# Kernel optimization log

Hardware: AMD Instinct MI355X
Metric: run time of the kernel (lower is better)

The kernel has to match this reference:

```python
import jax, jax.numpy as jnp
import numpy as np
import math

B, S, E, H = 2, 2048, 1024, 16
D = E // H          # d_k = 64 = n_qubits_per_head
F = 1024            # ffn_dim; MUST equal E for the original mixing to broadcast
LN_EPS = 1e-5


def _layernorm(x, g, b):
    m = jnp.mean(x, axis=-1, keepdims=True)
    v = jnp.var(x, axis=-1, keepdims=True)
    return (x - m) / jnp.sqrt(v + LN_EPS) * g + b


def _circuit_expvals(x):
    # Closed form of the variational circuit: RY(x_i) on wire i, RZ(theta_i),
    # CNOT chain (i -> i+1), measure PauliZ on each wire.
    # RZ is diagonal (no effect on Z probs); CNOT chain makes bit_i the XOR of
    # bits 0..i, so <Z_i> = prod_{j<=i} cos(x_j).
    return jnp.cumprod(jnp.cos(x), axis=-1)


def setup_inputs() -> dict:
    key = jax.random.key(0)
    ks = jax.random.split(key, 18)
    sc = 0.02
    inp = {
        "x": jax.random.normal(ks[0], (B, S, E), jnp.float32),
        "mask": jnp.ones((B, S), jnp.int32),
        "wq": jax.random.normal(ks[1], (E, E), jnp.float32) * sc,
        "wk": jax.random.normal(ks[2], (E, E), jnp.float32) * sc,
        "wv": jax.random.normal(ks[3], (E, E), jnp.float32) * sc,
        "wo": jax.random.normal(ks[4], (E, E), jnp.float32) * sc,
        "attn_param": jax.random.normal(ks[5], (D,), jnp.float32),   # RZ angles (no effect on expvals)
        "attn_qw": jnp.float32(0.5),
        "w1": jax.random.normal(ks[6], (E, F), jnp.float32) * sc,
        "b1": jnp.zeros((F,), jnp.float32),
        "w2": jax.random.normal(ks[7], (F, E), jnp.float32) * sc,
        "b2": jnp.zeros((E,), jnp.float32),
        "ffn_param": jax.random.normal(ks[8], (E,), jnp.float32),    # RZ angles (no effect on expvals)
        "ffn_qw": jnp.float32(0.5),
        "ln1_g": jnp.ones((E,), jnp.float32),
        "ln1_b": jnp.zeros((E,), jnp.float32),
        "ln2_g": jnp.ones((E,), jnp.float32),
        "ln2_b": jnp.zeros((E,), jnp.float32),
    }
    return inp


def reference(x, mask, wq, wk, wv, wo, attn_param, attn_qw,
              w1, b1, w2, b2, ffn_param, ffn_qw,
              ln1_g, ln1_b, ln2_g, ln2_b):
    b, s, _ = x.shape
    # ---- quantum attention sublayer (dropout inactive / eval mode) ----
    q = (x @ wq).reshape(b, s, H, D).transpose(0, 2, 1, 3)  # [b,h,s,d]
    k = (x @ wk).reshape(b, s, H, D).transpose(0, 2, 1, 3)
    v = (x @ wv).reshape(b, s, H, D).transpose(0, 2, 1, 3)
    scores = jnp.einsum("bhqd,bhkd->bhqk", q, k) / math.sqrt(D)
    scores = jnp.where(mask[:, None, None, :] == 0, -jnp.inf, scores)
    attn = jax.nn.softmax(scores, axis=-1)
    classical = jnp.einsum("bhqk,bhkd->bhqd", attn, v)
    quantum = _circuit_expvals(q)                             # [b,h,s,d]
    wgt = jax.nn.sigmoid(attn_qw)
    out = wgt * quantum + (1.0 - wgt) * classical
    attn_out = out.transpose(0, 2, 1, 3).reshape(b, s, E) @ wo
    x1 = _layernorm(x + attn_out, ln1_g, ln1_b)
    # ---- quantum feed-forward sublayer ----
    classical2 = jax.nn.relu(x1 @ w1 + b1)                    # [b,s,F]
    quantum2 = _circuit_expvals(x1)                           # [b,s,E] (E==F)
    wgt2 = jax.nn.sigmoid(ffn_qw)
    h = wgt2 * quantum2 + (1.0 - wgt2) * classical2
    ffn_out = h @ w2 + b2
    return _layernorm(x1 + ffn_out, ln2_g, ln2_b)
```

## Files before the change

### kernel.cpp

```cpp
#include <hip/hip_runtime.h>
#include <hip/hip_bf16.h>
#include <cmath>
#include <cstdint>


typedef __bf16 bf16_t;
typedef __bf16 bf16x8 __attribute__((ext_vector_type(8)));
typedef float f32x4 __attribute__((ext_vector_type(4)));
typedef unsigned short u16x4 __attribute__((ext_vector_type(4)));

#define DEV_INLINE __device__ __forceinline__
#define MB 1048576

DEV_INLINE void gload16(const void* g, void* lds) {
  __builtin_amdgcn_global_load_lds(
      (const __attribute__((address_space(1))) unsigned int*)g,
      (__attribute__((address_space(3))) unsigned int*)lds, 16, 0, 0);
}

DEV_INLINE unsigned short bf16_bits(float f) {
  bf16_t b = (bf16_t)f;
  return __builtin_bit_cast(unsigned short, b);
}

#define BAR_PRE_LGKM asm volatile("s_waitcnt lgkmcnt(0)" ::: "memory")
#define BAR_PRE_VM8 asm volatile("s_waitcnt vmcnt(8)" ::: "memory")
#define BAR_PRE_VM4 asm volatile("s_waitcnt vmcnt(4)" ::: "memory")
#define RAW_BAR                 \
  __builtin_amdgcn_s_barrier(); \
  asm volatile("" ::: "memory")

__global__ __launch_bounds__(256) void prep_kernel(
    const float* __restrict__ x, const float* __restrict__ wq,
    const float* __restrict__ wk, const float* __restrict__ wv,
    const float* __restrict__ wo, const float* __restrict__ w1,
    const float* __restrict__ w2, bf16_t* __restrict__ xc,
    bf16_t* __restrict__ wqkvT, bf16_t* __restrict__ wT3) {
  __shared__ bf16_t t[32][33];
  const int bid = blockIdx.x;
  if (bid < 2048) {
    const size_t i0 = ((size_t)bid * 256 + threadIdx.x) * 8;
    bf16x8 v;
#pragma unroll
    for (int j = 0; j < 8; ++j) v[j] = (bf16_t)x[i0 + j];
    *(bf16x8*)(xc + i0) = v;
    return;
  }
  const int grp = (bid - 2048) / 3072;
  const int tcb = (bid - 2048) - grp * 3072;
  const int mi = tcb >> 10;
  const float* src;
  bf16_t* dst;
  if (grp == 0) {
    src = (mi == 0) ? wq : (mi == 1) ? wk : wv;
    dst = wqkvT;
  } else {
    src = (mi == 0) ? wo : (mi == 1) ? w1 : w2;
    dst = wT3;
  }
  const int rem = tcb & 1023;
  const int bx = (rem & 31) * 32, by = (rem >> 5) * 32;
  const int tx = threadIdx.x & 31, ty = threadIdx.x >> 5;
#pragma unroll
  for (int i = 0; i < 4; ++i)
    t[ty + i * 8][tx] = (bf16_t)src[(size_t)(by + ty + i * 8) * 1024 + bx + tx];
  __syncthreads();
#pragma unroll
  for (int i = 0; i < 4; ++i)
    dst[(size_t)(mi * 1024 + bx + ty + i * 8) * 1024 + by + tx] = t[tx][ty + i * 8];
}

DEV_INLINE void stage_tile(const char* __restrict__ G, char* ldsT, int k0b,
                           int wid, int lane) {
#pragma unroll
  for (int t = 0; t < 4; ++t) {
    const int plin = t * 8192 + wid * 1024 + lane * 16;
    const int p = plin ^ ((((unsigned)plin >> 7) & 7) << 4);
    gload16(G + (size_t)(p >> 7) * 2048 + k0b + (p & 127),
            ldsT + t * 8192 + wid * 1024);
  }
}

DEV_INLINE void compute_tile(const char* lds_tile, int wm, int wn, int quad,
                             int tc, f32x4 (&acc)[8][4]) {
  const char* Ab = lds_tile;
  const char* Bb = lds_tile + 32768;
#pragma unroll
  for (int ks = 0; ks < 2; ++ks) {
    const int colb = ks * 64 + quad * 16;
    bf16x8 bfv[4];
#pragma unroll
    for (int j = 0; j < 4; ++j) {
      const int r = wn + j * 16 + tc;
      bfv[j] = *(const bf16x8*)(Bb + ((r * 128 + colb) ^ ((r & 7) << 4)));
    }
#pragma unroll
    for (int ih = 0; ih < 2; ++ih) {
      bf16x8 af[4];
#pragma unroll
      for (int i = 0; i < 4; ++i) {
        const int r = wm + (ih * 4 + i) * 16 + tc;
        af[i] = *(const bf16x8*)(Ab + ((r * 128 + colb) ^ ((r & 7) << 4)));
      }
      __builtin_amdgcn_s_setprio(1);
#pragma unroll
      for (int i = 0; i < 4; ++i)
#pragma unroll
        for (int j = 0; j < 4; ++j)
          acc[ih * 4 + i][j] = __builtin_amdgcn_mfma_f32_16x16x32_bf16(
              af[i], bfv[j], acc[ih * 4 + i][j], 0, 0, 0);
      __builtin_amdgcn_s_setprio(0);
    }
  }
}

__global__ __launch_bounds__(512, 2) void qkvvt8_kernel(
    const bf16_t* __restrict__ xc, const bf16_t* __restrict__ wqkvT,
    bf16_t* __restrict__ qb, bf16_t* __restrict__ kb,
    bf16_t* __restrict__ vTb) {
  __shared__ __align__(16) char lds[131072];
  const int tid = threadIdx.x, wid = tid >> 6, lane = tid & 63;
  const int quad = lane >> 4, tc = lane & 15;
  const int bid = blockIdx.x;
  const int isqk = (bid < 128);
  int m0, n0;
  const char *A, *B;
  if (isqk) {
    m0 = (bid >> 3) * 256;
    n0 = (bid & 7) * 256;
    A = (const char*)(xc + (size_t)m0 * 1024);
    B = (const char*)(wqkvT + (size_t)n0 * 1024);
  } else {
    const int t2 = bid - 128;
    m0 = (t2 >> 4) * 256;
    n0 = (t2 & 15) * 256;
    A = (const char*)(wqkvT + (size_t)(2 * 1024 * 1024) + (size_t)m0 * 1024);
    B = (const char*)(xc + (size_t)n0 * 1024);
  }
  const int wm = (wid >> 2) * 128, wn = (wid & 3) * 64;

  f32x4 acc[8][4] = {};

  stage_tile(A, lds, 0, wid, lane);
  stage_tile(B, lds + 32768, 0, wid, lane);
  stage_tile(A, lds + 65536, 128, wid, lane);
  stage_tile(B, lds + 98304, 128, wid, lane);
  BAR_PRE_VM8;
  RAW_BAR;

  for (int it = 0; it < 7; ++it) {
    const int k0b = it * 256 + 256;
    compute_tile(lds, wm, wn, quad, tc, acc);
    BAR_PRE_LGKM;
    RAW_BAR;
    stage_tile(A, lds, k0b, wid, lane);
    stage_tile(B, lds + 32768, k0b, wid, lane);
    BAR_PRE_VM8;
    RAW_BAR;
    compute_tile(lds + 65536, wm, wn, quad, tc, acc);
    BAR_PRE_LGKM;
    RAW_BAR;
    stage_tile(A, lds + 65536, k0b + 128, wid, lane);
    stage_tile(B, lds + 98304, k0b + 128, wid, lane);
    BAR_PRE_VM8;
    RAW_BAR;
  }
  compute_tile(lds, wm, wn, quad, tc, acc);
  asm volatile("s_waitcnt vmcnt(0)" ::: "memory");
  BAR_PRE_LGKM;
  RAW_BAR;
  compute_tile(lds + 65536, wm, wn, quad, tc, acc);

#pragma unroll
  for (int i = 0; i < 8; ++i) {
#pragma unroll
    for (int j = 0; j < 4; ++j) {
      const int row0 = m0 + wm + i * 16 + quad * 4;
      const int col = n0 + wn + j * 16 + tc;
      if (isqk) {
        const int part = col >> 10, e = col & 1023, hh = e >> 6, d = e & 63;
        bf16_t* dst = part ? kb : qb;
#pragma unroll
        for (int r = 0; r < 4; ++r) {
          const int row = row0 + r;
          const int b = row >> 11, s = row & 2047;
          dst[((size_t)(b * 16 + hh) * 2048 + s) * 64 + d] = (bf16_t)acc[i][j][r];
        }
      } else {
        const int b = col >> 11, s = col & 2047;
#pragma unroll
        for (int r = 0; r < 4; ++r) {
          vTb[((size_t)(b * 1024 + row0 + r)) * 2048 + s] = (bf16_t)acc[i][j][r];
        }
      }
    }
  }
}

enum { EPI_WO = 2, EPI_W1 = 3, EPI_W2 = 4 };

DEV_INLINE void stage128(const char* __restrict__ G, char* ldsT, int k0b,
                         int wid, int lane) {
#pragma unroll
  for (int t = 0; t < 4; ++t) {
    const int plin = t * 4096 + wid * 1024 + lane * 16;
    const int p = plin ^ ((((unsigned)plin >> 7) & 7) << 4);
    gload16(G + (size_t)(p >> 7) * 2048 + k0b + (p & 127),
            ldsT + t * 4096 + wid * 1024);
  }
}

DEV_INLINE void compute128(const char* lds_tile, int wm, int wn, int quad,
                           int tc, f32x4 (&acc)[4][4]) {
  const char* Ab = lds_tile;
  const char* Bb = lds_tile + 16384;
#pragma unroll
  for (int ks = 0; ks < 2; ++ks) {
    const int colb = ks * 64 + quad * 16;
    bf16x8 bfv[4];
#pragma unroll
    for (int j = 0; j < 4; ++j) {
      const int r = wn + j * 16 + tc;
      bfv[j] = *(const bf16x8*)(Bb + ((r * 128 + colb) ^ ((r & 7) << 4)));
    }
#pragma unroll
    for (int ih = 0; ih < 2; ++ih) {
      bf16x8 af[2];
#pragma unroll
      for (int i = 0; i < 2; ++i) {
        const int r = wm + (ih * 2 + i) * 16 + tc;
        af[i] = *(const bf16x8*)(Ab + ((r * 128 + colb) ^ ((r & 7) << 4)));
      }
      __builtin_amdgcn_s_setprio(1);
#pragma unroll
      for (int i = 0; i < 2; ++i)
#pragma unroll
        for (int j = 0; j < 4; ++j)
          acc[ih * 2 + i][j] = __builtin_amdgcn_mfma_f32_16x16x32_bf16(
              af[i], bfv[j], acc[ih * 2 + i][j], 0, 0, 0);
      __builtin_amdgcn_s_setprio(0);
    }
  }
}

template <int EPI>
__global__ __launch_bounds__(256, 2) void gemm8_kernel(
    const bf16_t* __restrict__ A, const bf16_t* __restrict__ Bt,
    void* __restrict__ o0, const float* __restrict__ auxf,
    const bf16_t* __restrict__ auxb, const float* __restrict__ bias,
    const float* __restrict__ scal) {
  __shared__ __align__(16) char lds[65536];
  const int tid = threadIdx.x, wid = tid >> 6, lane = tid & 63;
  const int quad = lane >> 4, tc = lane & 15;
  const int bid = blockIdx.x;
  const int g = (bid & 7) * 32 + (bid >> 3);
  const int m0 = (g >> 3) * 128, n0 = (g & 7) * 128;
  const char* Ag = (const char*)A + (size_t)m0 * 2048;
  const char* Bg = (const char*)Bt + (size_t)n0 * 2048;
  const int wm = (wid >> 1) * 64, wn = (wid & 1) * 64;

  f32x4 acc[4][4] = {};

  stage128(Ag, lds, 0, wid, lane);
  stage128(Bg, lds + 16384, 0, wid, lane);
  stage128(Ag, lds + 32768, 128, wid, lane);
  stage128(Bg, lds + 49152, 128, wid, lane);
  BAR_PRE_VM4;
  RAW_BAR;

  for (int it = 0; it < 7; ++it) {
    const int k0b = it * 256 + 256;
    compute128(lds, wm, wn, quad, tc, acc);
    BAR_PRE_LGKM;
    RAW_BAR;
    stage128(Ag, lds, k0b, wid, lane);
    stage128(Bg, lds + 16384, k0b, wid, lane);
    BAR_PRE_VM4;
    RAW_BAR;
    compute128(lds + 32768, wm, wn, quad, tc, acc);
    BAR_PRE_LGKM;
    RAW_BAR;
    stage128(Ag, lds + 32768, k0b + 128, wid, lane);
    stage128(Bg, lds + 49152, k0b + 128, wid, lane);
    BAR_PRE_VM4;
    RAW_BAR;
  }
  compute128(lds, wm, wn, quad, tc, acc);
  asm volatile("s_waitcnt vmcnt(0)" ::: "memory");
  BAR_PRE_LGKM;
  RAW_BAR;
  compute128(lds + 32768, wm, wn, quad, tc, acc);

  float wsig = 0.f;
  if (EPI == EPI_W1) wsig = 1.f / (1.f + __expf(-scal[0]));

#pragma unroll
  for (int i = 0; i < 4; ++i) {
#pragma unroll
    for (int j = 0; j < 4; ++j) {
      const int row0 = m0 + wm + i * 16 + quad * 4;
      const int col = n0 + wn + j * 16 + tc;
      if (EPI == EPI_WO) {
#pragma unroll
        for (int r = 0; r < 4; ++r) {
          const int row = row0 + r;
          ((float*)o0)[(size_t)row * 1024 + col] =
              acc[i][j][r] + auxf[(size_t)row * 1024 + col];
        }
      } else if (EPI == EPI_W1) {
#pragma unroll
        for (int r = 0; r < 4; ++r) {
          const int row = row0 + r;
          float c = fmaxf(acc[i][j][r] + bias[col], 0.f);
          const float qv = (float)auxb[(size_t)row * 1024 + col];
          ((bf16_t*)o0)[(size_t)row * 1024 + col] =
              (bf16_t)(wsig * qv + (1.f - wsig) * c);
        }
      } else {
#pragma unroll
        for (int r = 0; r < 4; ++r) {
          const int row = row0 + r;
          ((float*)o0)[(size_t)row * 1024 + col] =
              acc[i][j][r] + bias[col] + (float)auxb[(size_t)row * 1024 + col];
        }
      }
    }
  }
}

__global__ __launch_bounds__(256) void attn_kernel(
    const bf16_t* __restrict__ q, const bf16_t* __restrict__ k,
    const bf16_t* __restrict__ vT, const float* __restrict__ aqw,
    bf16_t* __restrict__ out) {
  constexpr int S = 2048, LDK = 72;
  __shared__ __align__(16) bf16_t Ks[64 * LDK];
  __shared__ __align__(16) bf16_t Vs[64 * LDK];
  __shared__ __align__(16) bf16_t Ps[4][32 * LDK];
  __shared__ bf16_t Ql[128 * LDK];
  __shared__ float segp[128][4];

  const int tid = threadIdx.x, w = tid >> 6, lane = tid & 63;
  const int quad = lane >> 4, tc = lane & 15;
  const int bh = blockIdx.y, q0 = blockIdx.x * 128;
  const bf16_t* qg = q + ((size_t)bh * S + q0) * 64;
  const bf16_t* kg = k + (size_t)bh * S * 64;
  const bf16_t* vg = vT + (size_t)bh * 64 * S;

  const int strow = tid >> 2, stcol = (tid & 3) * 16;

  bf16x8 pk0 = *(const bf16x8*)(kg + (size_t)strow * 64 + stcol);
  bf16x8 pk1 = *(const bf16x8*)(kg + (size_t)strow * 64 + stcol + 8);
  bf16x8 pv0 = *(const bf16x8*)(vg + (size_t)strow * S + stcol);
  bf16x8 pv1 = *(const bf16x8*)(vg + (size_t)strow * S + stcol + 8);

  {
    float c[2][16];
    const int ss = tid & 3;
#pragma unroll
    for (int pass = 0; pass < 2; ++pass) {
      const int rr = pass * 64 + (tid >> 2);
      const bf16_t* qr = qg + rr * 64 + ss * 16;
      float p = 1.f;
#pragma unroll
      for (int j2 = 0; j2 < 16; ++j2) {
        c[pass][j2] = __cosf((float)qr[j2]);
        p *= c[pass][j2];
      }
      segp[rr][ss] = p;
    }
    __syncthreads();
#pragma unroll
    for (int pass = 0; pass < 2; ++pass) {
      const int rr = pass * 64 + (tid >> 2);
      float pre = 1.f;
      for (int u = 0; u < ss; ++u) pre *= segp[rr][u];
#pragma unroll
      for (int j2 = 0; j2 < 16; ++j2) {
        pre *= c[pass][j2];
        Ql[rr * LDK + ss * 16 + j2] = (bf16_t)pre;
      }
    }
  }

  bf16x8 aq[2][2];
#pragma unroll
  for (int qs = 0; qs < 2; ++qs) {
    const int qrow = w * 32 + qs * 16 + tc;
#pragma unroll
    for (int ks = 0; ks < 2; ++ks) {
      bf16x8 t = *(const bf16x8*)(qg + qrow * 64 + ks * 32 + quad * 8);
#pragma unroll
      for (int e = 0; e < 8; ++e) t[e] = (bf16_t)((float)t[e] * 0.18033688f);
      aq[qs][ks] = t;
    }
  }

  float lacc[2] = {0.f, 0.f};
  f32x4 o[2][4] = {};
  bf16_t* Pw = Ps[w];

  for (int kt = 0; kt < S; kt += 64) {
    __syncthreads();
    *(bf16x8*)&Ks[strow * LDK + stcol] = pk0;
    *(bf16x8*)&Ks[strow * LDK + stcol + 8] = pk1;
    *(bf16x8*)&Vs[strow * LDK + stcol] = pv0;
    *(bf16x8*)&Vs[strow * LDK + stcol + 8] = pv1;
    if (kt + 64 < S) {
      const int nk = kt + 64;
      pk0 = *(const bf16x8*)(kg + (size_t)(nk + strow) * 64 + stcol);
      pk1 = *(const bf16x8*)(kg + (size_t)(nk + strow) * 64 + stcol + 8);
      pv0 = *(const bf16x8*)(vg + (size_t)strow * S + nk + stcol);
      pv1 = *(const bf16x8*)(vg + (size_t)strow * S + nk + stcol + 8);
    }
    __syncthreads();

    f32x4 sf[2][4] = {};
#pragma unroll
    for (int ks = 0; ks < 2; ++ks) {
#pragma unroll
      for (int nt = 0; nt < 4; ++nt) {
        bf16x8 ak = *(const bf16x8*)&Ks[(nt * 16 + tc) * LDK + ks * 32 + quad * 8];
        sf[0][nt] = __builtin_amdgcn_mfma_f32_16x16x32_bf16(ak, aq[0][ks], sf[0][nt], 0, 0, 0);
        sf[1][nt] = __builtin_amdgcn_mfma_f32_16x16x32_bf16(ak, aq[1][ks], sf[1][nt], 0, 0, 0);
      }
    }

#pragma unroll
    for (int qs = 0; qs < 2; ++qs) {
#pragma unroll
      for (int nt = 0; nt < 4; ++nt) {
        u16x4 pk;
        float ps = 0.f;
#pragma unroll
        for (int r = 0; r < 4; ++r) {
          const float p = __builtin_amdgcn_exp2f(sf[qs][nt][r]);
          ps += p;
          pk[r] = bf16_bits(p);
        }
        lacc[qs] += ps;
        *(u16x4*)&Pw[(qs * 16 + tc) * LDK + nt * 16 + quad * 4] = pk;
      }
    }
    asm volatile("s_waitcnt lgkmcnt(0)" ::: "memory");

#pragma unroll
    for (int ks = 0; ks < 2; ++ks) {
      bf16x8 ap0 = *(const bf16x8*)&Pw[tc * LDK + ks * 32 + quad * 8];
      bf16x8 ap1 = *(const bf16x8*)&Pw[(16 + tc) * LDK + ks * 32 + quad * 8];
#pragma unroll
      for (int j = 0; j < 4; ++j) {
        bf16x8 bv = *(const bf16x8*)&Vs[(j * 16 + tc) * LDK + ks * 32 + quad * 8];
        o[0][j] = __builtin_amdgcn_mfma_f32_16x16x32_bf16(ap0, bv, o[0][j], 0, 0, 0);
        o[1][j] = __builtin_amdgcn_mfma_f32_16x16x32_bf16(ap1, bv, o[1][j], 0, 0, 0);
      }
    }
  }

#pragma unroll
  for (int qs = 0; qs < 2; ++qs) {
    lacc[qs] += __shfl_xor(lacc[qs], 16, 64);
    lacc[qs] += __shfl_xor(lacc[qs], 32, 64);
  }

  const float wsig = 1.f / (1.f + __expf(-aqw[0]));
  const int b = bh >> 4, h = bh & 15;
#pragma unroll
  for (int qs = 0; qs < 2; ++qs) {
#pragma unroll
    for (int r = 0; r < 4; ++r) {
      const int lr = quad * 4 + r;
      const float linv = 1.f / __shfl(lacc[qs], lr, 64);
      const int lrow = w * 32 + qs * 16 + lr;
      const int sg = q0 + lrow;
#pragma unroll
      for (int j = 0; j < 4; ++j) {
        const int d = j * 16 + tc;
        const float cl = o[qs][j][r] * linv;
        const float qv = (float)Ql[lrow * LDK + d];
        out[((size_t)(b * 2048 + sg)) * 1024 + h * 64 + d] =
            (bf16_t)(wsig * qv + (1.f - wsig) * cl);
      }
    }
  }
}

__global__ __launch_bounds__(256) void ln1scan_kernel(
    const float* __restrict__ res, const float* __restrict__ g,
    const float* __restrict__ bta, bf16_t* __restrict__ x1,
    bf16_t* __restrict__ q2) {
  const int row = blockIdx.x;
  const int tid = threadIdx.x, w = tid >> 6, lane = tid & 63;
  f32x4 v = *(const f32x4*)&res[(size_t)row * 1024 + tid * 4];
  float s = v[0] + v[1] + v[2] + v[3];
  float sq = v[0] * v[0] + v[1] * v[1] + v[2] * v[2] + v[3] * v[3];
#pragma unroll
  for (int off = 32; off >= 1; off >>= 1) {
    s += __shfl_xor(s, off, 64);
    sq += __shfl_xor(sq, off, 64);
  }
  __shared__ float rs[4], rq[4], wtot[4];
  if (lane == 0) {
    rs[w] = s;
    rq[w] = sq;
  }
  __syncthreads();
  s = rs[0] + rs[1] + rs[2] + rs[3];
  sq = rq[0] + rq[1] + rq[2] + rq[3];
  const float mean = s * (1.f / 1024.f);
  const float var = fmaxf(sq * (1.f / 1024.f) - mean * mean, 0.f);
  const float rstd = rsqrtf(var + 1e-5f);

  const f32x4 gv = *(const f32x4*)&g[tid * 4];
  const f32x4 bv = *(const f32x4*)&bta[tid * 4];
  float c[4], p = 1.f;
  u16x4 xb;
#pragma unroll
  for (int i = 0; i < 4; ++i) {
    const float y = (v[i] - mean) * rstd * gv[i] + bv[i];
    const bf16_t yb = (bf16_t)y;
    xb[i] = __builtin_bit_cast(unsigned short, yb);
    c[i] = __cosf((float)yb);
    p *= c[i];
  }
  *(u16x4*)&x1[(size_t)row * 1024 + tid * 4] = xb;

  float ip = p;
#pragma unroll
  for (int off = 1; off < 64; off <<= 1) {
    const float t = __shfl_up(ip, off, 64);
    if (lane >= off) ip *= t;
  }
  if (lane == 63) wtot[w] = ip;
  __syncthreads();
  float carry = 1.f;
  for (int u = 0; u < w; ++u) carry *= wtot[u];
  float run = __shfl_up(ip, 1, 64);
  if (lane == 0) run = 1.f;
  run *= carry;
  u16x4 qv;
#pragma unroll
  for (int i = 0; i < 4; ++i) {
    run *= c[i];
    qv[i] = bf16_bits(run);
  }
  *(u16x4*)&q2[(size_t)row * 1024 + tid * 4] = qv;
}

__global__ __launch_bounds__(256) void ln2_kernel(
    const float* __restrict__ res, const float* __restrict__ g,
    const float* __restrict__ bta, float* __restrict__ out) {
  const int row = blockIdx.x;
  const int tid = threadIdx.x, w = tid >> 6, lane = tid & 63;
  f32x4 v = *(const f32x4*)&res[(size_t)row * 1024 + tid * 4];
  float s = v[0] + v[1] + v[2] + v[3];
  float sq = v[0] * v[0] + v[1] * v[1] + v[2] * v[2] + v[3] * v[3];
#pragma unroll
  for (int off = 32; off >= 1; off >>= 1) {
    s += __shfl_xor(s, off, 64);
    sq += __shfl_xor(sq, off, 64);
  }
  __shared__ float rs[4], rq[4];
  if (lane == 0) {
    rs[w] = s;
    rq[w] = sq;
  }
  __syncthreads();
  s = rs[0] + rs[1] + rs[2] + rs[3];
  sq = rq[0] + rq[1] + rq[2] + rq[3];
  const float mean = s * (1.f / 1024.f);
  const float var = fmaxf(sq * (1.f / 1024.f) - mean * mean, 0.f);
  const float rstd = rsqrtf(var + 1e-5f);
  const f32x4 gv = *(const f32x4*)&g[tid * 4];
  const f32x4 bv = *(const f32x4*)&bta[tid * 4];
  f32x4 y;
#pragma unroll
  for (int i = 0; i < 4; ++i) y[i] = (v[i] - mean) * rstd * gv[i] + bv[i];
  *(f32x4*)&out[(size_t)row * 1024 + tid * 4] = y;
}

extern "C" void kernel_launch(void* const* d_in, const int* in_sizes, int n_in,
                              void* d_out, int out_size, void* d_ws,
                              size_t ws_size, hipStream_t stream) {
  (void)in_sizes;
  (void)n_in;
  (void)out_size;
  (void)ws_size;
  const float* x = (const float*)d_in[0];
  const float* wq = (const float*)d_in[2];
  const float* wk = (const float*)d_in[3];
  const float* wv = (const float*)d_in[4];
  const float* wo = (const float*)d_in[5];
  const float* attn_qw = (const float*)d_in[7];
  const float* w1 = (const float*)d_in[8];
  const float* b1 = (const float*)d_in[9];
  const float* w2 = (const float*)d_in[10];
  const float* b2 = (const float*)d_in[11];
  const float* ffn_qw = (const float*)d_in[13];
  const float* ln1_g = (const float*)d_in[14];
  const float* ln1_b = (const float*)d_in[15];
  const float* ln2_g = (const float*)d_in[16];
  const float* ln2_b = (const float*)d_in[17];

  char* ws = (char*)d_ws;
  char* wsout = (char*)d_out;
  bf16_t* wT3 = (bf16_t*)(ws + 0);
  bf16_t* wqkvT = (bf16_t*)(ws + 6 * MB);
  bf16_t* xc = (bf16_t*)(ws + 12 * MB);
  bf16_t* qb = (bf16_t*)(ws + 20 * MB);
  bf16_t* aout = (bf16_t*)(ws + 6 * MB);
  float* res = (float*)(ws + 14 * MB);
  bf16_t* x1 = (bf16_t*)(ws + 6 * MB);
  float* res2 = (float*)(ws + 14 * MB);
  bf16_t* kb = (bf16_t*)(wsout + 0);
  bf16_t* vTb = (bf16_t*)(wsout + 8 * MB);
  bf16_t* q2 = (bf16_t*)(wsout + 0);
  bf16_t* hbuf = (bf16_t*)(wsout + 8 * MB);

  const dim3 tb(256);

  prep_kernel<<<8192, tb, 0, stream>>>(x, wq, wk, wv, wo, w1, w2, xc, wqkvT, wT3);

  qkvvt8_kernel<<<192, dim3(512), 0, stream>>>(xc, wqkvT, qb, kb, vTb);

  attn_kernel<<<dim3(16, 32), tb, 0, stream>>>(qb, kb, vTb, attn_qw, aout);

  gemm8_kernel<EPI_WO><<<256, tb, 0, stream>>>(
      aout, wT3, res, x, nullptr, nullptr, nullptr);

  ln1scan_kernel<<<4096, tb, 0, stream>>>(res, ln1_g, ln1_b, x1, q2);

  gemm8_kernel<EPI_W1><<<256, tb, 0, stream>>>(
      x1, wT3 + 1024 * 1024, hbuf, nullptr, q2, b1, ffn_qw);

  gemm8_kernel<EPI_W2><<<256, tb, 0, stream>>>(
      hbuf, wT3 + 2 * 1024 * 1024, res2, nullptr, x1, b2, nullptr);

  ln2_kernel<<<4096, tb, 0, stream>>>(res2, ln2_g, ln2_b, (float*)d_out);
}
```

Measured before the change: 266.9 us.

## Split attention blocks into eight waves of 16 rows and compute cumprod via shuffles

```diff
diff --git a/kernel.cpp b/kernel.cpp
--- a/kernel.cpp
+++ b/kernel.cpp
@@ -328,16 +328,14 @@
   }
 }
 
-__global__ __launch_bounds__(256) void attn_kernel(
+__global__ __launch_bounds__(512, 4) void attn_kernel(
     const bf16_t* __restrict__ q, const bf16_t* __restrict__ k,
     const bf16_t* __restrict__ vT, const float* __restrict__ aqw,
     bf16_t* __restrict__ out) {
   constexpr int S = 2048, LDK = 72;
   __shared__ __align__(16) bf16_t Ks[64 * LDK];
   __shared__ __align__(16) bf16_t Vs[64 * LDK];
-  __shared__ __align__(16) bf16_t Ps[4][32 * LDK];
-  __shared__ bf16_t Ql[128 * LDK];
-  __shared__ float segp[128][4];
+  __shared__ __align__(16) bf16_t Ps[8][16 * LDK];
 
   const int tid = threadIdx.x, w = tid >> 6, lane = tid & 63;
   const int quad = lane >> 4, tc = lane & 15;
@@ -346,140 +344,107 @@
   const bf16_t* kg = k + (size_t)bh * S * 64;
   const bf16_t* vg = vT + (size_t)bh * 64 * S;
 
-  const int strow = tid >> 2, stcol = (tid & 3) * 16;
-
-  bf16x8 pk0 = *(const bf16x8*)(kg + (size_t)strow * 64 + stcol);
-  bf16x8 pk1 = *(const bf16x8*)(kg + (size_t)strow * 64 + stcol + 8);
-  bf16x8 pv0 = *(const bf16x8*)(vg + (size_t)strow * S + stcol);
-  bf16x8 pv1 = *(const bf16x8*)(vg + (size_t)strow * S + stcol + 8);
-
-  {
-    float c[2][16];
-    const int ss = tid & 3;
-#pragma unroll
-    for (int pass = 0; pass < 2; ++pass) {
-      const int rr = pass * 64 + (tid >> 2);
-      const bf16_t* qr = qg + rr * 64 + ss * 16;
-      float p = 1.f;
-#pragma unroll
-      for (int j2 = 0; j2 < 16; ++j2) {
-        c[pass][j2] = __cosf((float)qr[j2]);
-        p *= c[pass][j2];
-      }
-      segp[rr][ss] = p;
-    }
-    __syncthreads();
-#pragma unroll
-    for (int pass = 0; pass < 2; ++pass) {
-      const int rr = pass * 64 + (tid >> 2);
-      float pre = 1.f;
-      for (int u = 0; u < ss; ++u) pre *= segp[rr][u];
-#pragma unroll
-      for (int j2 = 0; j2 < 16; ++j2) {
-        pre *= c[pass][j2];
-        Ql[rr * LDK + ss * 16 + j2] = (bf16_t)pre;
-      }
-    }
-  }
-
-  bf16x8 aq[2][2];
-#pragma unroll
-  for (int qs = 0; qs < 2; ++qs) {
-    const int qrow = w * 32 + qs * 16 + tc;
-#pragma unroll
-    for (int ks = 0; ks < 2; ++ks) {
-      bf16x8 t = *(const bf16x8*)(qg + qrow * 64 + ks * 32 + quad * 8);
-#pragma unroll
-      for (int e = 0; e < 8; ++e) t[e] = (bf16_t)((float)t[e] * 0.18033688f);
-      aq[qs][ks] = t;
-    }
-  }
-
-  float lacc[2] = {0.f, 0.f};
-  f32x4 o[2][4] = {};
+  const int strow = tid >> 3, stcol = (tid & 7) * 8;
+
+  bf16x8 pk = *(const bf16x8*)(kg + (size_t)strow * 64 + stcol);
+  bf16x8 pv = *(const bf16x8*)(vg + (size_t)strow * S + stcol);
+
+  bf16x8 aq[2];
+  const int qrow = w * 16 + tc;
+#pragma unroll
+  for (int ks = 0; ks < 2; ++ks) {
+    bf16x8 t = *(const bf16x8*)(qg + qrow * 64 + ks * 32 + quad * 8);
+#pragma unroll
+    for (int e = 0; e < 8; ++e) t[e] = (bf16_t)((float)t[e] * 0.18033688f);
+    aq[ks] = t;
+  }
+
+  float lacc = 0.f;
+  f32x4 o[4] = {};
   bf16_t* Pw = Ps[w];
 
   for (int kt = 0; kt < S; kt += 64) {
     __syncthreads();
-    *(bf16x8*)&Ks[strow * LDK + stcol] = pk0;
-    *(bf16x8*)&Ks[strow * LDK + stcol + 8] = pk1;
-    *(bf16x8*)&Vs[strow * LDK + stcol] = pv0;
-    *(bf16x8*)&Vs[strow * LDK + stcol + 8] = pv1;
+    *(bf16x8*)&Ks[strow * LDK + stcol] = pk;
+    *(bf16x8*)&Vs[strow * LDK + stcol] = pv;
     if (kt + 64 < S) {
       const int nk = kt + 64;
-      pk0 = *(const bf16x8*)(kg + (size_t)(nk + strow) * 64 + stcol);
-      pk1 = *(const bf16x8*)(kg + (size_t)(nk + strow) * 64 + stcol + 8);
-      pv0 = *(const bf16x8*)(vg + (size_t)strow * S + nk + stcol);
-      pv1 = *(const bf16x8*)(vg + (size_t)strow * S + nk + stcol + 8);
+      pk = *(const bf16x8*)(kg + (size_t)(nk + strow) * 64 + stcol);
+      pv = *(const bf16x8*)(vg + (size_t)strow * S + nk + stcol);
     }
     __syncthreads();
 
-    f32x4 sf[2][4] = {};
+    f32x4 sf[4] = {};
 #pragma unroll
     for (int ks = 0; ks < 2; ++ks) {
 #pragma unroll
       for (int nt = 0; nt < 4; ++nt) {
         bf16x8 ak = *(const bf16x8*)&Ks[(nt * 16 + tc) * LDK + ks * 32 + quad * 8];
-        sf[0][nt] = __builtin_amdgcn_mfma_f32_16x16x32_bf16(ak, aq[0][ks], sf[0][nt], 0, 0, 0);
-        sf[1][nt] = __builtin_amdgcn_mfma_f32_16x16x32_bf16(ak, aq[1][ks], sf[1][nt], 0, 0, 0);
-      }
-    }
-
-#pragma unroll
-    for (int qs = 0; qs < 2; ++qs) {
-#pragma unroll
-      for (int nt = 0; nt < 4; ++nt) {
-        u16x4 pk;
-        float ps = 0.f;
-#pragma unroll
-        for (int r = 0; r < 4; ++r) {
-          const float p = __builtin_amdgcn_exp2f(sf[qs][nt][r]);
-          ps += p;
-          pk[r] = bf16_bits(p);
-        }
-        lacc[qs] += ps;
-        *(u16x4*)&Pw[(qs * 16 + tc) * LDK + nt * 16 + quad * 4] = pk;
-      }
+        sf[nt] = __builtin_amdgcn_mfma_f32_16x16x32_bf16(ak, aq[ks], sf[nt], 0, 0, 0);
+      }
+    }
+
+#pragma unroll
+    for (int nt = 0; nt < 4; ++nt) {
+      u16x4 pkk;
+      float ps = 0.f;
+#pragma unroll
+      for (int r = 0; r < 4; ++r) {
+        const float p = __builtin_amdgcn_exp2f(sf[nt][r]);
+        ps += p;
+        pkk[r] = bf16_bits(p);
+      }
+      lacc += ps;
+      *(u16x4*)&Pw[tc * LDK + nt * 16 + quad * 4] = pkk;
     }
     asm volatile("s_waitcnt lgkmcnt(0)" ::: "memory");
 
 #pragma unroll
     for (int ks = 0; ks < 2; ++ks) {
-      bf16x8 ap0 = *(const bf16x8*)&Pw[tc * LDK + ks * 32 + quad * 8];
-      bf16x8 ap1 = *(const bf16x8*)&Pw[(16 + tc) * LDK + ks * 32 + quad * 8];
+      bf16x8 ap = *(const bf16x8*)&Pw[tc * LDK + ks * 32 + quad * 8];
 #pragma unroll
       for (int j = 0; j < 4; ++j) {
         bf16x8 bv = *(const bf16x8*)&Vs[(j * 16 + tc) * LDK + ks * 32 + quad * 8];
-        o[0][j] = __builtin_amdgcn_mfma_f32_16x16x32_bf16(ap0, bv, o[0][j], 0, 0, 0);
-        o[1][j] = __builtin_amdgcn_mfma_f32_16x16x32_bf16(ap1, bv, o[1][j], 0, 0, 0);
-      }
-    }
-  }
-
-#pragma unroll
-  for (int qs = 0; qs < 2; ++qs) {
-    lacc[qs] += __shfl_xor(lacc[qs], 16, 64);
-    lacc[qs] += __shfl_xor(lacc[qs], 32, 64);
-  }
+        o[j] = __builtin_amdgcn_mfma_f32_16x16x32_bf16(ap, bv, o[j], 0, 0, 0);
+      }
+    }
+  }
+
+  lacc += __shfl_xor(lacc, 16, 64);
+  lacc += __shfl_xor(lacc, 32, 64);
 
   const float wsig = 1.f / (1.f + __expf(-aqw[0]));
   const int b = bh >> 4, h = bh & 15;
 #pragma unroll
-  for (int qs = 0; qs < 2; ++qs) {
-#pragma unroll
-    for (int r = 0; r < 4; ++r) {
-      const int lr = quad * 4 + r;
-      const float linv = 1.f / __shfl(lacc[qs], lr, 64);
-      const int lrow = w * 32 + qs * 16 + lr;
-      const int sg = q0 + lrow;
+  for (int r = 0; r < 4; ++r) {
+    const int lr = quad * 4 + r;
+    const float linv = 1.f / __shfl(lacc, lr, 64);
+    const int lrow = w * 16 + lr;
+    const int sg = q0 + lrow;
+
+    float qv[4];
+    {
+      float gprod = 1.f;
 #pragma unroll
       for (int j = 0; j < 4; ++j) {
-        const int d = j * 16 + tc;
-        const float cl = o[qs][j][r] * linv;
-        const float qv = (float)Ql[lrow * LDK + d];
-        out[((size_t)(b * 2048 + sg)) * 1024 + h * 64 + d] =
-            (bf16_t)(wsig * qv + (1.f - wsig) * cl);
-      }
+        float pp = __cosf((float)qg[(size_t)lrow * 64 + j * 16 + tc]);
+#pragma unroll
+        for (int off = 1; off < 16; off <<= 1) {
+          const float t = __shfl_up(pp, off, 64);
+          if (tc >= off) pp *= t;
+        }
+        const float Gj = __shfl(pp, (lane & 48) + 15, 64);
+        qv[j] = gprod * pp;
+        gprod *= Gj;
+      }
+    }
+
+#pragma unroll
+    for (int j = 0; j < 4; ++j) {
+      const int d = j * 16 + tc;
+      const float cl = o[j][r] * linv;
+      out[((size_t)(b * 2048 + sg)) * 1024 + h * 64 + d] =
+          (bf16_t)(wsig * qv[j] + (1.f - wsig) * cl);
     }
   }
 }
@@ -622,7 +587,7 @@
 
   qkvvt8_kernel<<<192, dim3(512), 0, stream>>>(xc, wqkvT, qb, kb, vTb);
 
-  attn_kernel<<<dim3(16, 32), tb, 0, stream>>>(qb, kb, vTb, attn_qw, aout);
+  attn_kernel<<<dim3(16, 32), dim3(512), 0, stream>>>(qb, kb, vTb, attn_qw, aout);
 
   gemm8_kernel<EPI_WO><<<256, tb, 0, stream>>>(
       aout, wT3, res, x, nullptr, nullptr, nullptr);
```

Measured after the change: 274.2 us. +2.7%, slower.

## Restructure QKV GEMM mainloop into 8-phase quadrant pipeline with finer-grained staging

Applied to the files above, without the earlier changes.

```diff
diff --git a/kernel.cpp b/kernel.cpp
--- a/kernel.cpp
+++ b/kernel.cpp
@@ -24,11 +24,22 @@
 }
 
 #define BAR_PRE_LGKM asm volatile("s_waitcnt lgkmcnt(0)" ::: "memory")
-#define BAR_PRE_VM8 asm volatile("s_waitcnt vmcnt(8)" ::: "memory")
 #define BAR_PRE_VM4 asm volatile("s_waitcnt vmcnt(4)" ::: "memory")
 #define RAW_BAR                 \
   __builtin_amdgcn_s_barrier(); \
   asm volatile("" ::: "memory")
+
+template <int N>
+DEV_INLINE void waitvm() {
+  if constexpr (N == 6)
+    asm volatile("s_waitcnt vmcnt(6)" ::: "memory");
+  else if constexpr (N == 4)
+    asm volatile("s_waitcnt vmcnt(4)" ::: "memory");
+  else if constexpr (N == 2)
+    asm volatile("s_waitcnt vmcnt(2)" ::: "memory");
+  else
+    asm volatile("s_waitcnt vmcnt(0)" ::: "memory");
+}
 
 __global__ __launch_bounds__(256) void prep_kernel(
     const float* __restrict__ x, const float* __restrict__ wq,
@@ -70,48 +81,63 @@
     dst[(size_t)(mi * 1024 + bx + ty + i * 8) * 1024 + by + tx] = t[tx][ty + i * 8];
 }
 
-DEV_INLINE void stage_tile(const char* __restrict__ G, char* ldsT, int k0b,
-                           int wid, int lane) {
-#pragma unroll
-  for (int t = 0; t < 4; ++t) {
-    const int plin = t * 8192 + wid * 1024 + lane * 16;
+DEV_INLINE void stage_unit(int g, const char* __restrict__ A,
+                           const char* __restrict__ B, char* lds, int wid,
+                           int tid) {
+  const int tau = g >> 2, u = g & 3;
+  char* region = lds + (tau & 1) * 65536 + ((u & 1) ? 32768 : 0) +
+                 ((u >> 1) ? 16384 : 0);
+  const char* Gb = ((u & 1) ? B : A) + (size_t)((u >> 1) * 128) * 2048;
+  const int k0b = tau * 128;
+#pragma unroll
+  for (int t = 0; t < 2; ++t) {
+    const int plin = t * 8192 + tid * 16;
     const int p = plin ^ ((((unsigned)plin >> 7) & 7) << 4);
-    gload16(G + (size_t)(p >> 7) * 2048 + k0b + (p & 127),
-            ldsT + t * 8192 + wid * 1024);
-  }
-}
-
-DEV_INLINE void compute_tile(const char* lds_tile, int wm, int wn, int quad,
-                             int tc, f32x4 (&acc)[8][4]) {
-  const char* Ab = lds_tile;
-  const char* Bb = lds_tile + 32768;
+    gload16(Gb + (size_t)(p >> 7) * 2048 + k0b + (p & 127),
+            region + t * 8192 + (tid >> 6) * 1024);
+  }
+}
+
+template <int P, bool DO_STAGE, int VMN>
+DEV_INLINE void do_phase(char* lds, const char* __restrict__ Ag,
+                         const char* __restrict__ Bg, int g, int wid, int tid,
+                         int wrow, int wcol, int quad, int tc,
+                         f32x4 (&acc)[2][2][4][2]) {
+  constexpr int q = P & 3, buf = P >> 2;
+  constexpr int ha = q >> 1, hb = q & 1;
+  const char* Ar = lds + buf * 65536 + ha * 16384;
+  const char* Br = lds + buf * 65536 + 32768 + hb * 16384;
+  bf16x8 af[2][4], bfv[2][2];
 #pragma unroll
   for (int ks = 0; ks < 2; ++ks) {
     const int colb = ks * 64 + quad * 16;
-    bf16x8 bfv[4];
-#pragma unroll
-    for (int j = 0; j < 4; ++j) {
-      const int r = wn + j * 16 + tc;
-      bfv[j] = *(const bf16x8*)(Bb + ((r * 128 + colb) ^ ((r & 7) << 4)));
-    }
-#pragma unroll
-    for (int ih = 0; ih < 2; ++ih) {
-      bf16x8 af[4];
-#pragma unroll
-      for (int i = 0; i < 4; ++i) {
-        const int r = wm + (ih * 4 + i) * 16 + tc;
-        af[i] = *(const bf16x8*)(Ab + ((r * 128 + colb) ^ ((r & 7) << 4)));
-      }
-      __builtin_amdgcn_s_setprio(1);
-#pragma unroll
-      for (int i = 0; i < 4; ++i)
-#pragma unroll
-        for (int j = 0; j < 4; ++j)
-          acc[ih * 4 + i][j] = __builtin_amdgcn_mfma_f32_16x16x32_bf16(
-              af[i], bfv[j], acc[ih * 4 + i][j], 0, 0, 0);
-      __builtin_amdgcn_s_setprio(0);
-    }
-  }
+#pragma unroll
+    for (int cf = 0; cf < 2; ++cf) {
+      const int r = wcol + cf * 16 + tc;
+      bfv[ks][cf] = *(const bf16x8*)(Br + ((r * 128 + colb) ^ ((r & 7) << 4)));
+    }
+#pragma unroll
+    for (int rf = 0; rf < 4; ++rf) {
+      const int r = wrow + rf * 16 + tc;
+      af[ks][rf] = *(const bf16x8*)(Ar + ((r * 128 + colb) ^ ((r & 7) << 4)));
+    }
+  }
+  if constexpr (DO_STAGE) stage_unit(g, Ag, Bg, lds, wid, tid);
+  waitvm<VMN>();
+  __builtin_amdgcn_s_barrier();
+  asm volatile("s_waitcnt lgkmcnt(0)" ::: "memory");
+  __builtin_amdgcn_s_setprio(1);
+#pragma unroll
+  for (int ks = 0; ks < 2; ++ks)
+#pragma unroll
+    for (int rf = 0; rf < 4; ++rf)
+#pragma unroll
+      for (int cf = 0; cf < 2; ++cf)
+        acc[ha][hb][rf][cf] = __builtin_amdgcn_mfma_f32_16x16x32_bf16(
+            af[ks][rf], bfv[ks][cf], acc[ha][hb][rf][cf], 0, 0, 0);
+  __builtin_amdgcn_s_setprio(0);
+  __builtin_amdgcn_s_barrier();
+  asm volatile("" ::: "memory");
 }
 
 __global__ __launch_bounds__(512, 2) void qkvvt8_kernel(
@@ -124,73 +150,77 @@
   const int bid = blockIdx.x;
   const int isqk = (bid < 128);
   int m0, n0;
-  const char *A, *B;
+  const char *Ag, *Bg;
   if (isqk) {
     m0 = (bid >> 3) * 256;
     n0 = (bid & 7) * 256;
-    A = (const char*)(xc + (size_t)m0 * 1024);
-    B = (const char*)(wqkvT + (size_t)n0 * 1024);
+    Ag = (const char*)(xc + (size_t)m0 * 1024);
+    Bg = (const char*)(wqkvT + (size_t)n0 * 1024);
   } else {
     const int t2 = bid - 128;
     m0 = (t2 >> 4) * 256;
     n0 = (t2 & 15) * 256;
-    A = (const char*)(wqkvT + (size_t)(2 * 1024 * 1024) + (size_t)m0 * 1024);
-    B = (const char*)(xc + (size_t)n0 * 1024);
-  }
-  const int wm = (wid >> 2) * 128, wn = (wid & 3) * 64;
-
-  f32x4 acc[8][4] = {};
-
-  stage_tile(A, lds, 0, wid, lane);
-  stage_tile(B, lds + 32768, 0, wid, lane);
-  stage_tile(A, lds + 65536, 128, wid, lane);
-  stage_tile(B, lds + 98304, 128, wid, lane);
-  BAR_PRE_VM8;
+    Ag = (const char*)(wqkvT + (size_t)(2 * 1024 * 1024) + (size_t)m0 * 1024);
+    Bg = (const char*)(xc + (size_t)n0 * 1024);
+  }
+  const int wrow = (wid >> 2) * 64;
+  const int wcol = (wid & 3) * 32;
+
+  f32x4 acc[2][2][4][2] = {};
+
+#pragma unroll
+  for (int g = 0; g < 6; ++g) stage_unit(g, Ag, Bg, lds, wid, tid);
+  waitvm<6>();
   RAW_BAR;
 
-  for (int it = 0; it < 7; ++it) {
-    const int k0b = it * 256 + 256;
-    compute_tile(lds, wm, wn, quad, tc, acc);
-    BAR_PRE_LGKM;
-    RAW_BAR;
-    stage_tile(A, lds, k0b, wid, lane);
-    stage_tile(B, lds + 32768, k0b, wid, lane);
-    BAR_PRE_VM8;
-    RAW_BAR;
-    compute_tile(lds + 65536, wm, wn, quad, tc, acc);
-    BAR_PRE_LGKM;
-    RAW_BAR;
-    stage_tile(A, lds + 65536, k0b + 128, wid, lane);
-    stage_tile(B, lds + 98304, k0b + 128, wid, lane);
-    BAR_PRE_VM8;
-    RAW_BAR;
-  }
-  compute_tile(lds, wm, wn, quad, tc, acc);
-  asm volatile("s_waitcnt vmcnt(0)" ::: "memory");
-  BAR_PRE_LGKM;
-  RAW_BAR;
-  compute_tile(lds + 65536, wm, wn, quad, tc, acc);
-
-#pragma unroll
-  for (int i = 0; i < 8; ++i) {
-#pragma unroll
-    for (int j = 0; j < 4; ++j) {
-      const int row0 = m0 + wm + i * 16 + quad * 4;
-      const int col = n0 + wn + j * 16 + tc;
-      if (isqk) {
-        const int part = col >> 10, e = col & 1023, hh = e >> 6, d = e & 63;
-        bf16_t* dst = part ? kb : qb;
-#pragma unroll
-        for (int r = 0; r < 4; ++r) {
-          const int row = row0 + r;
-          const int b = row >> 11, s = row & 2047;
-          dst[((size_t)(b * 16 + hh) * 2048 + s) * 64 + d] = (bf16_t)acc[i][j][r];
-        }
-      } else {
-        const int b = col >> 11, s = col & 2047;
-#pragma unroll
-        for (int r = 0; r < 4; ++r) {
-          vTb[((size_t)(b * 1024 + row0 + r)) * 2048 + s] = (bf16_t)acc[i][j][r];
+  for (int I = 0; I < 7; ++I) {
+    const int gb = 8 * I + 6;
+    do_phase<0, true, 6>(lds, Ag, Bg, gb + 0, wid, tid, wrow, wcol, quad, tc, acc);
+    do_phase<1, true, 6>(lds, Ag, Bg, gb + 1, wid, tid, wrow, wcol, quad, tc, acc);
+    do_phase<2, true, 6>(lds, Ag, Bg, gb + 2, wid, tid, wrow, wcol, quad, tc, acc);
+    do_phase<3, true, 6>(lds, Ag, Bg, gb + 3, wid, tid, wrow, wcol, quad, tc, acc);
+    do_phase<4, true, 6>(lds, Ag, Bg, gb + 4, wid, tid, wrow, wcol, quad, tc, acc);
+    do_phase<5, true, 6>(lds, Ag, Bg, gb + 5, wid, tid, wrow, wcol, quad, tc, acc);
+    do_phase<6, true, 6>(lds, Ag, Bg, gb + 6, wid, tid, wrow, wcol, quad, tc, acc);
+    do_phase<7, true, 6>(lds, Ag, Bg, gb + 7, wid, tid, wrow, wcol, quad, tc, acc);
+  }
+  do_phase<0, true, 6>(lds, Ag, Bg, 62, wid, tid, wrow, wcol, quad, tc, acc);
+  do_phase<1, true, 6>(lds, Ag, Bg, 63, wid, tid, wrow, wcol, quad, tc, acc);
+  do_phase<2, false, 4>(lds, Ag, Bg, 0, wid, tid, wrow, wcol, quad, tc, acc);
+  do_phase<3, false, 2>(lds, Ag, Bg, 0, wid, tid, wrow, wcol, quad, tc, acc);
+  do_phase<4, false, 0>(lds, Ag, Bg, 0, wid, tid, wrow, wcol, quad, tc, acc);
+  do_phase<5, false, 0>(lds, Ag, Bg, 0, wid, tid, wrow, wcol, quad, tc, acc);
+  do_phase<6, false, 0>(lds, Ag, Bg, 0, wid, tid, wrow, wcol, quad, tc, acc);
+  do_phase<7, false, 0>(lds, Ag, Bg, 0, wid, tid, wrow, wcol, quad, tc, acc);
+
+#pragma unroll
+  for (int ha = 0; ha < 2; ++ha) {
+#pragma unroll
+    for (int hb = 0; hb < 2; ++hb) {
+#pragma unroll
+      for (int rf = 0; rf < 4; ++rf) {
+#pragma unroll
+        for (int cf = 0; cf < 2; ++cf) {
+          const int row0 = m0 + ha * 128 + wrow + rf * 16 + quad * 4;
+          const int col = n0 + hb * 128 + wcol + cf * 16 + tc;
+          if (isqk) {
+            const int part = col >> 10, e = col & 1023, hh = e >> 6, d = e & 63;
+            bf16_t* dst = part ? kb : qb;
+#pragma unroll
+            for (int r = 0; r < 4; ++r) {
+              const int row = row0 + r;
+              const int b = row >> 11, s = row & 2047;
+              dst[((size_t)(b * 16 + hh) * 2048 + s) * 64 + d] =
+                  (bf16_t)acc[ha][hb][rf][cf][r];
+            }
+          } else {
+            const int b = col >> 11, s = col & 2047;
+#pragma unroll
+            for (int r = 0; r < 4; ++r) {
+              vTb[((size_t)(b * 1024 + row0 + r)) * 2048 + s] =
+                  (bf16_t)acc[ha][hb][rf][cf][r];
+            }
+          }
         }
       }
     }
```

Result: no change. 271.9 us (+1.9%).

## Double attention KV tile to 128 keys and compute quantum cumprod via shuffles

Applied to the files above, without the earlier changes.

```diff
diff --git a/kernel.cpp b/kernel.cpp
--- a/kernel.cpp
+++ b/kernel.cpp
@@ -332,12 +332,10 @@
     const bf16_t* __restrict__ q, const bf16_t* __restrict__ k,
     const bf16_t* __restrict__ vT, const float* __restrict__ aqw,
     bf16_t* __restrict__ out) {
-  constexpr int S = 2048, LDK = 72;
-  __shared__ __align__(16) bf16_t Ks[64 * LDK];
-  __shared__ __align__(16) bf16_t Vs[64 * LDK];
-  __shared__ __align__(16) bf16_t Ps[4][32 * LDK];
-  __shared__ bf16_t Ql[128 * LDK];
-  __shared__ float segp[128][4];
+  constexpr int S = 2048, LDK = 72, LDV = 136, LDP = 136;
+  __shared__ __align__(16) bf16_t Ks[128 * LDK];
+  __shared__ __align__(16) bf16_t Vs[64 * LDV];
+  __shared__ __align__(16) bf16_t Ps[4][32 * LDP];
 
   const int tid = threadIdx.x, w = tid >> 6, lane = tid & 63;
   const int quad = lane >> 4, tc = lane & 15;
@@ -346,40 +344,14 @@
   const bf16_t* kg = k + (size_t)bh * S * 64;
   const bf16_t* vg = vT + (size_t)bh * 64 * S;
 
-  const int strow = tid >> 2, stcol = (tid & 3) * 16;
-
-  bf16x8 pk0 = *(const bf16x8*)(kg + (size_t)strow * 64 + stcol);
-  bf16x8 pk1 = *(const bf16x8*)(kg + (size_t)strow * 64 + stcol + 8);
-  bf16x8 pv0 = *(const bf16x8*)(vg + (size_t)strow * S + stcol);
-  bf16x8 pv1 = *(const bf16x8*)(vg + (size_t)strow * S + stcol + 8);
-
-  {
-    float c[2][16];
-    const int ss = tid & 3;
-#pragma unroll
-    for (int pass = 0; pass < 2; ++pass) {
-      const int rr = pass * 64 + (tid >> 2);
-      const bf16_t* qr = qg + rr * 64 + ss * 16;
-      float p = 1.f;
-#pragma unroll
-      for (int j2 = 0; j2 < 16; ++j2) {
-        c[pass][j2] = __cosf((float)qr[j2]);
-        p *= c[pass][j2];
-      }
-      segp[rr][ss] = p;
-    }
-    __syncthreads();
-#pragma unroll
-    for (int pass = 0; pass < 2; ++pass) {
-      const int rr = pass * 64 + (tid >> 2);
-      float pre = 1.f;
-      for (int u = 0; u < ss; ++u) pre *= segp[rr][u];
-#pragma unroll
-      for (int j2 = 0; j2 < 16; ++j2) {
-        pre *= c[pass][j2];
-        Ql[rr * LDK + ss * 16 + j2] = (bf16_t)pre;
-      }
-    }
+  const int krow = tid >> 3, kcol = (tid & 7) * 8;
+  const int vrow = tid >> 4, vcol = (tid & 15) * 8;
+
+  bf16x8 pk[4], pv[4];
+#pragma unroll
+  for (int u = 0; u < 4; ++u) {
+    pk[u] = *(const bf16x8*)(kg + (size_t)(u * 32 + krow) * 64 + kcol);
+    pv[u] = *(const bf16x8*)(vg + (size_t)(u * 16 + vrow) * S + vcol);
   }
 
   bf16x8 aq[2][2];
@@ -399,26 +371,28 @@
   f32x4 o[2][4] = {};
   bf16_t* Pw = Ps[w];
 
-  for (int kt = 0; kt < S; kt += 64) {
+  for (int kt = 0; kt < S; kt += 128) {
     __syncthreads();
-    *(bf16x8*)&Ks[strow * LDK + stcol] = pk0;
-    *(bf16x8*)&Ks[strow * LDK + stcol + 8] = pk1;
-    *(bf16x8*)&Vs[strow * LDK + stcol] = pv0;
-    *(bf16x8*)&Vs[strow * LDK + stcol + 8] = pv1;
-    if (kt + 64 < S) {
-      const int nk = kt + 64;
-      pk0 = *(const bf16x8*)(kg + (size_t)(nk + strow) * 64 + stcol);
-      pk1 = *(const bf16x8*)(kg + (size_t)(nk + strow) * 64 + stcol + 8);
-      pv0 = *(const bf16x8*)(vg + (size_t)strow * S + nk + stcol);
-      pv1 = *(const bf16x8*)(vg + (size_t)strow * S + nk + stcol + 8);
+#pragma unroll
+    for (int u = 0; u < 4; ++u) {
+      *(bf16x8*)&Ks[(u * 32 + krow) * LDK + kcol] = pk[u];
+      *(bf16x8*)&Vs[(u * 16 + vrow) * LDV + vcol] = pv[u];
+    }
+    if (kt + 128 < S) {
+      const int nk = kt + 128;
+#pragma unroll
+      for (int u = 0; u < 4; ++u) {
+        pk[u] = *(const bf16x8*)(kg + (size_t)(nk + u * 32 + krow) * 64 + kcol);
+        pv[u] = *(const bf16x8*)(vg + (size_t)(u * 16 + vrow) * S + nk + vcol);
+      }
     }
     __syncthreads();
 
-    f32x4 sf[2][4] = {};
+    f32x4 sf[2][8] = {};
 #pragma unroll
     for (int ks = 0; ks < 2; ++ks) {
 #pragma unroll
-      for (int nt = 0; nt < 4; ++nt) {
+      for (int nt = 0; nt < 8; ++nt) {
         bf16x8 ak = *(const bf16x8*)&Ks[(nt * 16 + tc) * LDK + ks * 32 + quad * 8];
         sf[0][nt] = __builtin_amdgcn_mfma_f32_16x16x32_bf16(ak, aq[0][ks], sf[0][nt], 0, 0, 0);
         sf[1][nt] = __builtin_amdgcn_mfma_f32_16x16x32_bf16(ak, aq[1][ks], sf[1][nt], 0, 0, 0);
@@ -428,28 +402,28 @@
 #pragma unroll
     for (int qs = 0; qs < 2; ++qs) {
 #pragma unroll
-      for (int nt = 0; nt < 4; ++nt) {
-        u16x4 pk;
+      for (int nt = 0; nt < 8; ++nt) {
+        u16x4 pkk;
         float ps = 0.f;
 #pragma unroll
         for (int r = 0; r < 4; ++r) {
           const float p = __builtin_amdgcn_exp2f(sf[qs][nt][r]);
           ps += p;
-          pk[r] = bf16_bits(p);
+          pkk[r] = bf16_bits(p);
         }
         lacc[qs] += ps;
-        *(u16x4*)&Pw[(qs * 16 + tc) * LDK + nt * 16 + quad * 4] = pk;
+        *(u16x4*)&Pw[(qs * 16 + tc) * LDP + nt * 16 + quad * 4] = pkk;
       }
     }
     asm volatile("s_waitcnt lgkmcnt(0)" ::: "memory");
 
 #pragma unroll
-    for (int ks = 0; ks < 2; ++ks) {
-      bf16x8 ap0 = *(const bf16x8*)&Pw[tc * LDK + ks * 32 + quad * 8];
-      bf16x8 ap1 = *(const bf16x8*)&Pw[(16 + tc) * LDK + ks * 32 + quad * 8];
+    for (int ks = 0; ks < 4; ++ks) {
+      bf16x8 ap0 = *(const bf16x8*)&Pw[tc * LDP + ks * 32 + quad * 8];
+      bf16x8 ap1 = *(const bf16x8*)&Pw[(16 + tc) * LDP + ks * 32 + quad * 8];
 #pragma unroll
       for (int j = 0; j < 4; ++j) {
-        bf16x8 bv = *(const bf16x8*)&Vs[(j * 16 + tc) * LDK + ks * 32 + quad * 8];
+        bf16x8 bv = *(const bf16x8*)&Vs[(j * 16 + tc) * LDV + ks * 32 + quad * 8];
         o[0][j] = __builtin_amdgcn_mfma_f32_16x16x32_bf16(ap0, bv, o[0][j], 0, 0, 0);
         o[1][j] = __builtin_amdgcn_mfma_f32_16x16x32_bf16(ap1, bv, o[1][j], 0, 0, 0);
       }
@@ -472,13 +446,30 @@
       const float linv = 1.f / __shfl(lacc[qs], lr, 64);
       const int lrow = w * 32 + qs * 16 + lr;
       const int sg = q0 + lrow;
+
+      float qv[4];
+      {
+        float gprod = 1.f;
+#pragma unroll
+        for (int j = 0; j < 4; ++j) {
+          float pp = __cosf((float)qg[(size_t)lrow * 64 + j * 16 + tc]);
+#pragma unroll
+          for (int off = 1; off < 16; off <<= 1) {
+            const float t = __shfl_up(pp, off, 64);
+            if (tc >= off) pp *= t;
+          }
+          const float Gj = __shfl(pp, (lane & 48) + 15, 64);
+          qv[j] = gprod * pp;
+          gprod *= Gj;
+        }
+      }
+
 #pragma unroll
       for (int j = 0; j < 4; ++j) {
         const int d = j * 16 + tc;
         const float cl = o[qs][j][r] * linv;
-        const float qv = (float)Ql[lrow * LDK + d];
         out[((size_t)(b * 2048 + sg)) * 1024 + h * 64 + d] =
-            (bf16_t)(wsig * qv + (1.f - wsig) * cl);
+            (bf16_t)(wsig * qv[j] + (1.f - wsig) * cl);
       }
     }
   }
```

Result: slower. 274.4 us (+2.8%).
